# Optimization experiments

Measured on AMD Instinct MI355X. Metric: run time of the kernel, lower is better.

## Reference

```python
import jax, jax.numpy as jnp
import numpy as np

NUM_HEADS = 10
LN_EPS = 1e-5

def setup_inputs() -> dict:
    key = jax.random.key(0)
    ks = jax.random.split(key, 8)
    B, H, N, D, Dt = 256, 200, 64, 640, 256
    s = 0.02
    return {
        'clicked_news': jax.random.normal(ks[0], (B, H, D), jnp.float32),
        'clicked_topics': jax.random.normal(ks[1], (B, H, Dt), jnp.float32),
        'cand_topics': jax.random.normal(ks[2], (B, N, Dt), jnp.float32),
        'Wq': jax.random.normal(ks[3], (D, Dt), jnp.float32) * s,
        'bq': jnp.zeros((D,), jnp.float32),
        'Wk': jax.random.normal(ks[4], (D, Dt), jnp.float32) * s,
        'bk': jnp.zeros((D,), jnp.float32),
        'Wv': jax.random.normal(ks[5], (D, D), jnp.float32) * s,
        'bv': jnp.zeros((D,), jnp.float32),
        'Wg': jax.random.normal(ks[6], (D, D), jnp.float32) * s,
        'bg': jnp.zeros((D,), jnp.float32),
        'ln_gamma': jnp.ones((D,), jnp.float32),
        'ln_beta': jnp.zeros((D,), jnp.float32),
    }

def reference(clicked_news, clicked_topics, cand_topics, Wq, bq, Wk, bk, Wv, bv, Wg, bg, ln_gamma, ln_beta):
    B, H, D = clicked_news.shape
    N = cand_topics.shape[1]
    nh = NUM_HEADS
    hd = D // nh
    scale = jnp.sqrt(jnp.asarray(D, clicked_news.dtype))

    Qf = cand_topics @ Wq.T + bq            # [B, N, D]
    Kf = clicked_topics @ Wk.T + bk         # [B, H, D]
    # V projection feeds `weighted`, which is dead code w.r.t. outputs; omitted.

    Q = Qf.reshape(B, N, nh, hd)
    K = Kf.reshape(B, H, nh, hd)
    scores = jnp.einsum('bnhd,bmhd->bhnm', Q, K) / scale   # [B, nh, N, H]
    attn = jax.nn.softmax(scores, axis=-1)                 # dropout is identity in eval

    # query weighting: softmax over candidates of ||Q||
    query_weights = jax.nn.softmax(jnp.linalg.norm(Qf, axis=-1), axis=1)   # [B, N]
    agg = (attn.sum(axis=1) * query_weights[:, :, None]).sum(axis=1)       # [B, H]
    attn_weights_agg = jax.nn.softmax(agg, axis=-1)                        # [B, H]

    weighted_clicked = attn_weights_agg[:, :, None] * clicked_news         # [B, H, D]
    gate = jax.nn.sigmoid(weighted_clicked @ Wg.T + bg)
    out = gate * weighted_clicked + (1.0 - gate) * clicked_news

    mu = out.mean(axis=-1, keepdims=True)
    var = out.var(axis=-1, keepdims=True)
    out = (out - mu) / jnp.sqrt(var + LN_EPS) * ln_gamma + ln_beta
    return out, attn_weights_agg
```

## Files before the change

kernel.cpp:

```cpp
#include <hip/hip_runtime.h>
#include <math.h>

#define B_  256
#define H_  200
#define N_  64
#define D_  640
#define DT_ 256
#define NH_ 10
#define HD_ 64
#define MT_ 13
#define MH_ 25600

typedef __attribute__((ext_vector_type(8))) short bf16x8;
typedef __attribute__((ext_vector_type(4))) float f32x4;

__device__ __forceinline__ float wave_reduce_sum(float v) {
    #pragma unroll
    for (int m = 32; m > 0; m >>= 1) v += __shfl_xor(v, m);
    return v;
}
__device__ __forceinline__ float wave_reduce_max(float v) {
    #pragma unroll
    for (int m = 32; m > 0; m >>= 1) v = fmaxf(v, __shfl_xor(v, m));
    return v;
}
__device__ __forceinline__ float red16_sum(float v) {
    #pragma unroll
    for (int m = 1; m < 16; m <<= 1) v += __shfl_xor(v, m);
    return v;
}
__device__ __forceinline__ float red16_max(float v) {
    #pragma unroll
    for (int m = 1; m < 16; m <<= 1) v = fmaxf(v, __shfl_xor(v, m));
    return v;
}
__device__ __forceinline__ short f2bf(float x) {
    unsigned u = __float_as_uint(x);
    unsigned r = (u + 0x7fffu + ((u >> 16) & 1u)) >> 16;
    return (short)r;
}
__device__ __forceinline__ float bf2f(short s) {
    return __uint_as_float(((unsigned)(unsigned short)s) << 16);
}

__device__ __forceinline__ void gload_lds16(const void* g, void* lds) {
    __builtin_amdgcn_global_load_lds(
        (const __attribute__((address_space(1))) void*)g,
        (__attribute__((address_space(3))) void*)lds, 16, 0, 0);
}

__global__ __launch_bounds__(256) void convert3(
    const float* __restrict__ s0, short* __restrict__ d0, int n0,
    const float* __restrict__ s1, short* __restrict__ d1, int n1,
    const float* __restrict__ s2, short* __restrict__ d2, int n2)
{
    const int total = n0 + n1 + n2;
    for (int i = blockIdx.x * 256 + threadIdx.x; i < total; i += gridDim.x * 256) {
        if (i < n0)            d0[i] = f2bf(s0[i]);
        else if (i < n0 + n1)  d1[i - n0] = f2bf(s1[i - n0]);
        else                   d2[i - n0 - n1] = f2bf(s2[i - n0 - n1]);
    }
}

__global__ __launch_bounds__(256, 5) void gemm_bt(
    const float* __restrict__ A, int lda,
    const short* __restrict__ Wb, int ldb,
    const float* __restrict__ bias,
    short* __restrict__ Y, int nkc,
    float* __restrict__ qss)
{
    __shared__ float A_f[64 * 64];
    __shared__ short B_lds[128 * 64];
    const int t = threadIdx.x;
    const int lane = t & 63, w = t >> 6;
    const int wm = w >> 1, wn = w & 1;
    const int r16 = lane & 15, g = lane >> 4;
    const int lb = (blockIdx.x & 7) * ((int)gridDim.x >> 3) + (blockIdx.x >> 3);
    const int row0 = (lb / 5) * 64;
    const int col0 = (lb % 5) * 128;

    f32x4 acc[4][2];
    #pragma unroll
    for (int ct = 0; ct < 4; ++ct) {
        acc[ct][0] = (f32x4){0.f,0.f,0.f,0.f};
        acc[ct][1] = (f32x4){0.f,0.f,0.f,0.f};
    }

    for (int k = 0; k < nkc; ++k) {
        const int k0 = k * 64;
        #pragma unroll
        for (int j = 0; j < 4; ++j) {
            const int u = t + j * 256;
            const int row = u >> 4, jj = u & 15;
            gload_lds16(A + (long)(row0 + row) * lda + k0 + ((jj ^ (row & 7)) << 2),
                        (char*)A_f + u * 16);
        }
        #pragma unroll
        for (int j = 0; j < 4; ++j) {
            const int u = t + j * 256;
            const int col = u >> 3, jj = u & 7;
            gload_lds16(Wb + (long)(col0 + col) * ldb + k0 + ((jj ^ (col & 7)) << 3),
                        (char*)B_lds + u * 16);
        }
        __syncthreads();

        #pragma unroll
        for (int kk = 0; kk < 2; ++kk) {
            bf16x8 a[2];
            #pragma unroll
            for (int rt = 0; rt < 2; ++rt) {
                const int row = wm * 32 + rt * 16 + r16;
                const int s = kk * 8 + g * 2;
                float4 f0 = *(const float4*)(A_f + row * 64 + ((s ^ (row & 7)) << 2));
                float4 f1 = *(const float4*)(A_f + row * 64 + (((s + 1) ^ (row & 7)) << 2));
                bf16x8 av;
                av[0] = f2bf(f0.x); av[1] = f2bf(f0.y); av[2] = f2bf(f0.z); av[3] = f2bf(f0.w);
                av[4] = f2bf(f1.x); av[5] = f2bf(f1.y); av[6] = f2bf(f1.z); av[7] = f2bf(f1.w);
                a[rt] = av;
            }
            #pragma unroll
            for (int ct = 0; ct < 4; ++ct) {
                const int col = wn * 64 + ct * 16 + r16;
                const int sb = kk * 4 + g;
                bf16x8 b = *(const bf16x8*)(B_lds + col * 64 + ((sb ^ (col & 7)) << 3));
                acc[ct][0] = __builtin_amdgcn_mfma_f32_16x16x32_bf16(a[0], b, acc[ct][0], 0, 0, 0);
                acc[ct][1] = __builtin_amdgcn_mfma_f32_16x16x32_bf16(a[1], b, acc[ct][1], 0, 0, 0);
            }
        }
        __syncthreads();
    }

    float ps[2][4];
    #pragma unroll
    for (int rt = 0; rt < 2; ++rt)
        #pragma unroll
        for (int i = 0; i < 4; ++i) ps[rt][i] = 0.f;

    #pragma unroll
    for (int ct = 0; ct < 4; ++ct) {
        const int col = col0 + wn * 64 + ct * 16 + r16;
        const float bv = bias ? bias[col] : 0.f;
        #pragma unroll
        for (int rt = 0; rt < 2; ++rt)
            #pragma unroll
            for (int i = 0; i < 4; ++i) {
                const short ob = f2bf(acc[ct][rt][i] + bv);
                Y[(long)(row0 + wm * 32 + rt * 16 + g * 4 + i) * D_ + col] = ob;
                if (qss) { const float of = bf2f(ob); ps[rt][i] += of * of; }
            }
    }
    if (qss) {
        const int strip = col0 >> 7;
        #pragma unroll
        for (int rt = 0; rt < 2; ++rt)
            #pragma unroll
            for (int i = 0; i < 4; ++i) {
                const float s = red16_sum(ps[rt][i]);
                if (r16 == 0) {
                    const int row = row0 + wm * 32 + rt * 16 + g * 4 + i;
                    qss[(long)row * 10 + strip * 2 + wn] = s;
                }
            }
    }
}

__global__ __launch_bounds__(512, 2) void attn2(
    const short* __restrict__ Qb, const short* __restrict__ Kb,
    const float* __restrict__ qss,
    float* __restrict__ aw, float* __restrict__ out_tail)
{
    __shared__ short K_l[2][2][208 * 64];
    __shared__ float qw_l[N_];
    __shared__ float aggp[8][MT_ * 16];
    __shared__ float red2[2];
    const int t = threadIdx.x;
    const int lane = t & 63, w = t >> 6;
    const int wm = w & 3, hh = w >> 2;
    const int r16 = lane & 15, g = lane >> 4;
    const int b = blockIdx.x;
    const int tt = t & 255;
    const int half = t >> 8;

    auto STAGE_K = [&](int bi, int hi) {
        const int h = half * 5 + hi;
        #pragma unroll
        for (int j = 0; j < 7; ++j) {
            const int u = tt + j * 256;
            if (u < 208 * 8) {
                const int row = u >> 3, jg = u & 7;
                gload_lds16(Kb + ((long)(b * H_) + row) * D_ + h * HD_ +
                                ((jg ^ (row & 7)) << 3),
                            (char*)K_l[half][bi] + u * 16);
            }
        }
    };

    STAGE_K(0, 0);

    if (w == 0) {
        const float* qp = qss + ((long)(b * N_ + lane)) * 10;
        float ss = 0.f;
        #pragma unroll
        for (int j = 0; j < 10; ++j) ss += qp[j];
        float v = sqrtf(ss);
        float mx = wave_reduce_max(v);
        float e = __expf(v - mx);
        float s = wave_reduce_sum(e);
        qw_l[lane] = e / s;
    }
    __syncthreads();

    float qwr[4];
    #pragma unroll
    for (int i = 0; i < 4; ++i) qwr[i] = qw_l[wm * 16 + g * 4 + i];

    const float inv_scale = 0.0395284707521047f;
    float aggl[MT_];
    #pragma unroll
    for (int mt = 0; mt < MT_; ++mt) aggl[mt] = 0.f;

    for (int hi = 0; hi < 5; ++hi) {
        const int h = hh * 5 + hi;
        if (hi + 1 < 5) STAGE_K((hi + 1) & 1, hi + 1);

        const short* kl = K_l[hh][hi & 1];
        const short* qbase = Qb + ((long)(b * N_ + wm * 16 + r16)) * D_ + h * HD_ + g * 8;
        bf16x8 a0 = *(const bf16x8*)(qbase);
        bf16x8 a1 = *(const bf16x8*)(qbase + 32);
        bf16x8 kb0[MT_], kb1[MT_];
        #pragma unroll
        for (int mt = 0; mt < MT_; ++mt) {
            const int row = mt * 16 + r16;
            const int s0 = g ^ (row & 7);
            const int s1 = (g + 4) ^ (row & 7);
            kb0[mt] = *(const bf16x8*)(kl + row * 64 + s0 * 8);
            kb1[mt] = *(const bf16x8*)(kl + row * 64 + s1 * 8);
        }
        f32x4 acc[MT_];
        #pragma unroll
        for (int mt = 0; mt < MT_; ++mt) {
            f32x4 z = {0.f,0.f,0.f,0.f};
            z = __builtin_amdgcn_mfma_f32_16x16x32_bf16(a0, kb0[mt], z, 0, 0, 0);
            z = __builtin_amdgcn_mfma_f32_16x16x32_bf16(a1, kb1[mt], z, 0, 0, 0);
            acc[mt] = z;
        }
        const bool tailok = (r16 < 8);
        float mx[4] = {-INFINITY, -INFINITY, -INFINITY, -INFINITY};
        #pragma unroll
        for (int mt = 0; mt < MT_; ++mt) {
            const bool valid = (mt < 12) || tailok;
            #pragma unroll
            for (int i = 0; i < 4; ++i)
                if (valid) mx[i] = fmaxf(mx[i], acc[mt][i]);
        }
        #pragma unroll
        for (int i = 0; i < 4; ++i) mx[i] = red16_max(mx[i]);
        float sum[4] = {0.f, 0.f, 0.f, 0.f};
        #pragma unroll
        for (int mt = 0; mt < MT_; ++mt) {
            const bool valid = (mt < 12) || tailok;
            #pragma unroll
            for (int i = 0; i < 4; ++i) {
                float e = valid ? __expf((acc[mt][i] - mx[i]) * inv_scale) : 0.f;
                acc[mt][i] = e;
                sum[i] += e;
            }
        }
        float fct[4];
        #pragma unroll
        for (int i = 0; i < 4; ++i) fct[i] = qwr[i] / red16_sum(sum[i]);
        #pragma unroll
        for (int mt = 0; mt < MT_; ++mt)
            aggl[mt] += acc[mt][0] * fct[0] + acc[mt][1] * fct[1]
                      + acc[mt][2] * fct[2] + acc[mt][3] * fct[3];

        __syncthreads();
    }

    #pragma unroll
    for (int mt = 0; mt < MT_; ++mt) {
        aggl[mt] += __shfl_xor(aggl[mt], 16);
        aggl[mt] += __shfl_xor(aggl[mt], 32);
    }
    if (g == 0) {
        #pragma unroll
        for (int mt = 0; mt < MT_; ++mt) aggp[w][mt * 16 + r16] = aggl[mt];
    }
    __syncthreads();
    if (t < MT_ * 16) {
        float v = 0.f;
        #pragma unroll
        for (int j = 0; j < 8; ++j) v += aggp[j][t];
        aggp[0][t] = v;
    }
    __syncthreads();
    if (w == 0) {
        float v0 = aggp[0][lane], v1 = aggp[0][lane + 64], v2 = aggp[0][lane + 128];
        const bool has3 = lane < (H_ - 192);
        float v3 = has3 ? aggp[0][lane + 192] : -INFINITY;
        float mx = wave_reduce_max(fmaxf(fmaxf(v0, v1), fmaxf(v2, v3)));
        float s = __expf(v0 - mx) + __expf(v1 - mx) + __expf(v2 - mx)
                + (has3 ? __expf(v3 - mx) : 0.f);
        s = wave_reduce_sum(s);
        if (lane == 0) { red2[0] = mx; red2[1] = s; }
    }
    __syncthreads();
    if (t < H_) {
        float v = __expf(aggp[0][t] - red2[0]) / red2[1];
        aw[b * H_ + t] = v;
        out_tail[b * H_ + t] = v;
    }
}

__global__ __launch_bounds__(256) void blendln(
    const float* __restrict__ cl, const short* __restrict__ Z,
    const float* __restrict__ aw, const float* __restrict__ bg,
    const float* __restrict__ gamma, const float* __restrict__ beta,
    float* __restrict__ out)
{
    const int t = threadIdx.x;
    const int lane = t & 63, w = t >> 6;
    const int row = blockIdx.x * 4 + w;
    const float awr = aw[row];
    const long base = (long)row * D_;

    float o[10];
    float s = 0.f, sq = 0.f;
    #pragma unroll
    for (int i = 0; i < 10; ++i) {
        const int col = lane + 64 * i;
        const float y = bf2f(Z[base + col]);
        const float c = cl[base + col];
        const float z = awr * y + bg[col];
        const float gt = 1.f / (1.f + __expf(-z));
        const float ov = c * (1.f + gt * (awr - 1.f));
        o[i] = ov; s += ov; sq += ov * ov;
    }
    s  = wave_reduce_sum(s);
    sq = wave_reduce_sum(sq);
    const float mu  = s * (1.f / D_);
    const float var = sq * (1.f / D_) - mu * mu;
    const float ri  = 1.0f / sqrtf(var + 1e-5f);
    #pragma unroll
    for (int i = 0; i < 10; ++i) {
        const int col = lane + 64 * i;
        out[base + col] = (o[i] - mu) * ri * gamma[col] + beta[col];
    }
}

extern "C" void kernel_launch(void* const* d_in, const int* in_sizes, int n_in,
                              void* d_out, int out_size, void* d_ws, size_t ws_size,
                              hipStream_t stream) {
    const float* clicked_news   = (const float*)d_in[0];
    const float* clicked_topics = (const float*)d_in[1];
    const float* cand_topics    = (const float*)d_in[2];
    const float* Wq = (const float*)d_in[3];
    const float* bq = (const float*)d_in[4];
    const float* Wk = (const float*)d_in[5];
    const float* bk = (const float*)d_in[6];
    const float* Wg = (const float*)d_in[9];
    const float* bg = (const float*)d_in[10];
    const float* ln_gamma = (const float*)d_in[11];
    const float* ln_beta  = (const float*)d_in[12];

    float* out = (float*)d_out;
    float* ws  = (float*)d_ws;

    float* aw   = ws;
    short* Wq_b = (short*)(aw + (long)B_ * H_);
    short* Wk_b = Wq_b + (long)D_ * DT_;
    short* Wg_b = Wk_b + (long)D_ * DT_;
    float* qss  = (float*)(Wg_b + (long)D_ * D_);
    short* Qb   = (short*)(qss + (long)B_ * N_ * 10);
    short* Z    = Qb;
    short* Kb = (short*)d_out;
    float* out_tail = out + (long)B_ * H_ * D_;

    convert3<<<1440, 256, 0, stream>>>(Wq, Wq_b, D_ * DT_,
                                       Wk, Wk_b, D_ * DT_,
                                       Wg, Wg_b, D_ * D_);

    gemm_bt<<<1280, 256, 0, stream>>>(cand_topics, DT_, Wq_b, DT_, bq, Qb, 4, qss);
    gemm_bt<<<4000, 256, 0, stream>>>(clicked_topics, DT_, Wk_b, DT_, bk, Kb, 4, nullptr);
    attn2<<<B_, 512, 0, stream>>>(Qb, Kb, qss, aw, out_tail);

    for (int h = 0; h < 2; ++h) {
        const long off = (long)h * MH_;
        gemm_bt<<<2000, 256, 0, stream>>>(clicked_news + off * D_, D_,
                                          Wg_b, D_, nullptr, Z, 10, nullptr);
        blendln<<<MH_ / 4, 256, 0, stream>>>(
            clicked_news + off * D_, Z, aw + off, bg, ln_gamma, ln_beta,
            out + off * D_);
    }
}
```

Measured before the change: 265.9 us.

## Double-buffer LDS tiles in gemm_bt to overlap global loads with MFMA

Splits the A and B LDS tiles into two buffers and issues the async global-to-LDS loads for the next K chunk before computing the current one, waiting with explicit vmcnt counts and raw barriers. This is meant to hide global memory latency behind the MFMA work. LDS use doubles, so the launch-bounds occupancy hint drops from 5 to 2 blocks per CU. Fewer resident blocks may hide latency less well.

```diff
diff --git a/kernel.cpp b/kernel.cpp
--- a/kernel.cpp
+++ b/kernel.cpp
@@ -62,15 +62,15 @@
     }
 }
 
-__global__ __launch_bounds__(256, 5) void gemm_bt(
+__global__ __launch_bounds__(256, 2) void gemm_bt(
     const float* __restrict__ A, int lda,
     const short* __restrict__ Wb, int ldb,
     const float* __restrict__ bias,
     short* __restrict__ Y, int nkc,
     float* __restrict__ qss)
 {
-    __shared__ float A_f[64 * 64];
-    __shared__ short B_lds[128 * 64];
+    __shared__ float A_f[2][64 * 64];
+    __shared__ short B_l[2][128 * 64];
     const int t = threadIdx.x;
     const int lane = t & 63, w = t >> 6;
     const int wm = w >> 1, wn = w & 1;
@@ -86,24 +86,38 @@
         acc[ct][1] = (f32x4){0.f,0.f,0.f,0.f};
     }
 
-    for (int k = 0; k < nkc; ++k) {
+    auto STAGE = [&](int bi, int k) {
         const int k0 = k * 64;
         #pragma unroll
         for (int j = 0; j < 4; ++j) {
             const int u = t + j * 256;
             const int row = u >> 4, jj = u & 15;
             gload_lds16(A + (long)(row0 + row) * lda + k0 + ((jj ^ (row & 7)) << 2),
-                        (char*)A_f + u * 16);
+                        (char*)A_f[bi] + u * 16);
         }
         #pragma unroll
         for (int j = 0; j < 4; ++j) {
             const int u = t + j * 256;
             const int col = u >> 3, jj = u & 7;
             gload_lds16(Wb + (long)(col0 + col) * ldb + k0 + ((jj ^ (col & 7)) << 3),
-                        (char*)B_lds + u * 16);
-        }
-        __syncthreads();
-
+                        (char*)B_l[bi] + u * 16);
+        }
+    };
+
+    STAGE(0, 0);
+
+    for (int k = 0; k < nkc; ++k) {
+        if (k + 1 < nkc) {
+            STAGE((k + 1) & 1, k + 1);
+            asm volatile("s_waitcnt vmcnt(8)" ::: "memory");
+        } else {
+            asm volatile("s_waitcnt vmcnt(0)" ::: "memory");
+        }
+        __builtin_amdgcn_s_barrier();
+        __builtin_amdgcn_sched_barrier(0);
+
+        const float* ab = A_f[k & 1];
+        const short* bb = B_l[k & 1];
         #pragma unroll
         for (int kk = 0; kk < 2; ++kk) {
             bf16x8 a[2];
@@ -111,8 +125,8 @@
             for (int rt = 0; rt < 2; ++rt) {
                 const int row = wm * 32 + rt * 16 + r16;
                 const int s = kk * 8 + g * 2;
-                float4 f0 = *(const float4*)(A_f + row * 64 + ((s ^ (row & 7)) << 2));
-                float4 f1 = *(const float4*)(A_f + row * 64 + (((s + 1) ^ (row & 7)) << 2));
+                float4 f0 = *(const float4*)(ab + row * 64 + ((s ^ (row & 7)) << 2));
+                float4 f1 = *(const float4*)(ab + row * 64 + (((s + 1) ^ (row & 7)) << 2));
                 bf16x8 av;
                 av[0] = f2bf(f0.x); av[1] = f2bf(f0.y); av[2] = f2bf(f0.z); av[3] = f2bf(f0.w);
                 av[4] = f2bf(f1.x); av[5] = f2bf(f1.y); av[6] = f2bf(f1.z); av[7] = f2bf(f1.w);
@@ -122,12 +136,13 @@
             for (int ct = 0; ct < 4; ++ct) {
                 const int col = wn * 64 + ct * 16 + r16;
                 const int sb = kk * 4 + g;
-                bf16x8 b = *(const bf16x8*)(B_lds + col * 64 + ((sb ^ (col & 7)) << 3));
+                bf16x8 b = *(const bf16x8*)(bb + col * 64 + ((sb ^ (col & 7)) << 3));
                 acc[ct][0] = __builtin_amdgcn_mfma_f32_16x16x32_bf16(a[0], b, acc[ct][0], 0, 0, 0);
                 acc[ct][1] = __builtin_amdgcn_mfma_f32_16x16x32_bf16(a[1], b, acc[ct][1], 0, 0, 0);
             }
         }
-        __syncthreads();
+        __builtin_amdgcn_sched_barrier(0);
+        __builtin_amdgcn_s_barrier();
     }
 
     float ps[2][4];
```

After: 314.4 us. 1.18x slower.
